# Kernel tuning notes

Hardware: AMD Instinct MI355X
Metric: run time of the kernel (lower is better)

## Reference

```python
import jax, jax.numpy as jnp
import numpy as np

ALPHA = 0.2        # LeakyReLU negative slope
NEG_INF = -9e15    # mask value used by the torch module


def setup_inputs() -> dict:
    key = jax.random.key(0)
    ks = jax.random.split(key, 7)
    B, T, N, Cin = 4, 12, 1024, 64
    Fout, Em = 64, 16
    x = jax.random.normal(ks[0], (B, T, N, Cin), dtype=jnp.float32)
    adj = jax.random.randint(ks[1], (N, N), 0, 2, dtype=jnp.int32)
    emb1 = jax.random.normal(ks[2], (N, Em), dtype=jnp.float32)
    emb2 = jax.random.normal(ks[3], (N, Em), dtype=jnp.float32)
    W = jax.random.normal(ks[4], (Cin, Fout), dtype=jnp.float32) * (1.0 / np.sqrt(Cin))
    a = jax.random.normal(ks[5], (2 * Fout, 1), dtype=jnp.float32) * 0.1
    a2 = jax.random.normal(ks[6], (2 * Em, 1), dtype=jnp.float32) * 0.1
    return {"x": x, "adj": adj, "emb1": emb1, "emb2": emb2, "W": W, "a": a, "a2": a2}


def reference(x, adj, emb1, emb2, W, a, a2):
    B, T, N, Cin = x.shape
    Fout = W.shape[1]
    Em = emb1.shape[1]
    # Linear projection, fold batch*time: Wh [BT, N, Fout]
    Wh = jnp.einsum('btnc,cf->btnf', x, W).reshape(B * T, N, Fout)
    # Additive attention scores from node features
    s1 = Wh @ a[:Fout, 0]          # [BT, N]
    s2 = Wh @ a[Fout:, 0]          # [BT, N]
    e1 = s1[:, :, None] + s2[:, None, :]   # [BT, N, N]
    # Additive scores from static embeddings (shared across batch*time)
    f1 = emb1 @ a2[:Em, 0]         # [N]
    f2 = emb2 @ a2[Em:, 0]         # [N]
    e2 = f1[:, None] + f2[None, :]          # [N, N]
    e = jax.nn.leaky_relu(e1 + e2[None, :, :], negative_slope=ALPHA)
    # Adjacency mask + row softmax (dropout is inference no-op)
    att = jnp.where(adj[None, :, :] > 0, e, jnp.float32(NEG_INF))
    att = jax.nn.softmax(att, axis=-1)
    h_prime = att @ Wh                       # [BT, N, Fout]
    return jax.nn.elu(h_prime.reshape(B, T, N, Fout))
```

## Files before the change

kernel.cpp:

```cpp
#include <hip/hip_runtime.h>
#include <hip/hip_bf16.h>
#include <math.h>

#define BT 48
#define N 1024
#define F 64
#define CIN 64
#define EM 16
#define LRELU_A 0.2f
#define L2E 1.4426950408889634f

typedef short bf16x8 __attribute__((ext_vector_type(8)));
typedef float f32x4  __attribute__((ext_vector_type(4)));
typedef float f32x2  __attribute__((ext_vector_type(2)));
typedef float f32x4e __attribute__((ext_vector_type(4)));
typedef unsigned int u32x4 __attribute__((ext_vector_type(4)));

__device__ __forceinline__ unsigned short f2bf(float f) {
    unsigned int u = __float_as_uint(f);
    return (unsigned short)((u + 0x7FFFu + ((u >> 16) & 1u)) >> 16);
}

#define PKFMA(acc, xp, wp) \
    asm("v_pk_fma_f32 %0, %1, %2, %0" : "+v"(acc) : "v"(xp), "v"(wp))

__global__ __launch_bounds__(256) void k_proj_misc(
    const float* __restrict__ x, const float* __restrict__ W,
    const float* __restrict__ a,
    const int* __restrict__ adj,
    const float* __restrict__ emb1, const float* __restrict__ emb2,
    const float* __restrict__ a2,
    unsigned short* __restrict__ WhSw,
    float* __restrict__ s1, float* __restrict__ s2,
    unsigned int* __restrict__ adjBits,
    float* __restrict__ f1, float* __restrict__ f2)
{
    const int tid = threadIdx.x;
    const int b   = blockIdx.x;

    __shared__ __align__(16) float sxT[64 * 68];
    __shared__ __align__(16) float sW[64 * 68];

    const int bt  = b >> 4;
    const int n0  = (b & 15) * 64;
    const size_t grow = (size_t)bt * N + n0;

    {
        const float4* xv = (const float4*)(x + grow * CIN);
        for (int i = tid; i < 1024; i += 256) {
            const float4 v = xv[i];
            const int row = i >> 4, c4 = (i & 15) * 4;
            sxT[(c4 + 0) * 68 + (row ^ (((c4 + 0) & 15) << 2))] = v.x;
            sxT[(c4 + 1) * 68 + (row ^ (((c4 + 1) & 15) << 2))] = v.y;
            sxT[(c4 + 2) * 68 + (row ^ (((c4 + 2) & 15) << 2))] = v.z;
            sxT[(c4 + 3) * 68 + (row ^ (((c4 + 3) & 15) << 2))] = v.w;
        }
        const float4* wv = (const float4*)W;
        for (int i = tid; i < 1024; i += 256) {
            const int k = i >> 4, c4 = (i & 15) * 4;
            *(float4*)&sW[k * 68 + c4] = wv[i];
        }
    }
    __syncthreads();

    const int rg = tid >> 4, cg = tid & 15;
    const int r0 = rg * 4, c0 = cg * 4;

    f32x2 a00 = 0.f, a01 = 0.f, a10 = 0.f, a11 = 0.f;
    f32x2 a20 = 0.f, a21 = 0.f, a30 = 0.f, a31 = 0.f;

#pragma unroll
    for (int k = 0; k < CIN; ++k) {
        const float4 xr  = *(const float4*)&sxT[k * 68 + (r0 ^ ((k & 15) << 2))];
        const float4 wv4 = *(const float4*)&sW[k * 68 + c0];
        f32x2 w01; w01.x = wv4.x; w01.y = wv4.y;
        f32x2 w23; w23.x = wv4.z; w23.y = wv4.w;
        f32x2 xb;
        xb.x = xr.x; xb.y = xr.x;
        PKFMA(a00, xb, w01); PKFMA(a01, xb, w23);
        xb.x = xr.y; xb.y = xr.y;
        PKFMA(a10, xb, w01); PKFMA(a11, xb, w23);
        xb.x = xr.z; xb.y = xr.z;
        PKFMA(a20, xb, w01); PKFMA(a21, xb, w23);
        xb.x = xr.w; xb.y = xr.w;
        PKFMA(a30, xb, w01); PKFMA(a31, xb, w23);
    }

    {
        const float4 aw1 = *(const float4*)&a[c0];
        const float4 aw2 = *(const float4*)&a[F + c0];
        float v1r0 = a00.x*aw1.x + a00.y*aw1.y + a01.x*aw1.z + a01.y*aw1.w;
        float v1r1 = a10.x*aw1.x + a10.y*aw1.y + a11.x*aw1.z + a11.y*aw1.w;
        float v1r2 = a20.x*aw1.x + a20.y*aw1.y + a21.x*aw1.z + a21.y*aw1.w;
        float v1r3 = a30.x*aw1.x + a30.y*aw1.y + a31.x*aw1.z + a31.y*aw1.w;
        float v2r0 = a00.x*aw2.x + a00.y*aw2.y + a01.x*aw2.z + a01.y*aw2.w;
        float v2r1 = a10.x*aw2.x + a10.y*aw2.y + a11.x*aw2.z + a11.y*aw2.w;
        float v2r2 = a20.x*aw2.x + a20.y*aw2.y + a21.x*aw2.z + a21.y*aw2.w;
        float v2r3 = a30.x*aw2.x + a30.y*aw2.y + a31.x*aw2.z + a31.y*aw2.w;
#pragma unroll
        for (int off = 1; off <= 8; off <<= 1) {
            v1r0 += __shfl_xor(v1r0, off, 64); v2r0 += __shfl_xor(v2r0, off, 64);
            v1r1 += __shfl_xor(v1r1, off, 64); v2r1 += __shfl_xor(v2r1, off, 64);
            v1r2 += __shfl_xor(v1r2, off, 64); v2r2 += __shfl_xor(v2r2, off, 64);
            v1r3 += __shfl_xor(v1r3, off, 64); v2r3 += __shfl_xor(v2r3, off, 64);
        }
        if (cg == 0) {
            s1[grow + r0 + 0] = v1r0; s2[grow + r0 + 0] = v2r0;
            s1[grow + r0 + 1] = v1r1; s2[grow + r0 + 1] = v2r1;
            s1[grow + r0 + 2] = v1r2; s2[grow + r0 + 2] = v2r2;
            s1[grow + r0 + 3] = v1r3; s2[grow + r0 + 3] = v2r3;
        }
    }

    {
        const int nb = (b & 15) * 2 + (r0 >> 5);
        const int qq = (r0 >> 3) & 3;
        const int t0 = r0 & 7;
        const size_t base = ((size_t)(bt * 32 + nb) * 64) * 32;
#define STCOL(cc, v0, v1, v2, v3) do {                                      \
        const int c_ = c0 + (cc);                                           \
        const size_t off_ = base + (size_t)c_ * 32 + ((qq + c_) & 3) * 8 + t0; \
        ushort4 pv_;                                                        \
        pv_.x = f2bf(v0); pv_.y = f2bf(v1);                                 \
        pv_.z = f2bf(v2); pv_.w = f2bf(v3);                                 \
        *(ushort4*)&WhSw[off_] = pv_;                                       \
    } while (0)
        STCOL(0, a00.x, a10.x, a20.x, a30.x);
        STCOL(1, a00.y, a10.y, a20.y, a30.y);
        STCOL(2, a01.x, a11.x, a21.x, a31.x);
        STCOL(3, a01.y, a11.y, a21.y, a31.y);
#undef STCOL
    }

    if (b < 128) {
        const int idx = b * 256 + tid;
        const int r = idx >> 5, w32 = idx & 31;
        const int* p = adj + (size_t)r * N + w32 * 32;
        unsigned int m = 0;
#pragma unroll
        for (int j = 0; j < 32; ++j) m |= (p[j] > 0 ? 1u : 0u) << j;
        adjBits[idx] = m;
    } else if (b < 132) {
        const int n = (b - 128) * 256 + tid;
        float v1 = 0.f, v2 = 0.f;
#pragma unroll
        for (int k = 0; k < EM; ++k) {
            v1 = fmaf(emb1[n * EM + k], a2[k], v1);
            v2 = fmaf(emb2[n * EM + k], a2[EM + k], v2);
        }
        f1[n] = v1; f2[n] = v2;
    }
}


#define PAIRPK(x1p, x2p, bit, dest) do {                                   \
    f32x2 m1_, m2_;                                                        \
    asm("v_pk_mul_f32 %0, %1, %2" : "=v"(m1_) : "v"(x1p), "v"(E1p));       \
    asm("v_pk_mul_f32 %0, %1, %2" : "=v"(m2_) : "v"(x2p), "v"(E2p));       \
    float p0_ = fmaxf(m1_.x, m2_.x);                                       \
    float p1_ = fmaxf(m1_.y, m2_.y);                                       \
    p0_ = ((mb_ >> (bit)) & 1u) ? p0_ : 0.f;                               \
    p1_ = ((mb_ >> ((bit) + 1)) & 1u) ? p1_ : 0.f;                         \
    lsum += p0_ + p1_;                                                     \
    unsigned int pk_;                                                      \
    asm("v_cvt_pk_bf16_f32 %0, %1, %2" : "=v"(pk_) : "v"(p0_), "v"(p1_)); \
    dest = pk_;                                                            \
} while (0)

#define MAKE_ONE(ch, ks, Avar, abword) do {                                \
    const int jb_ = (ch) * 128 + (ks) * 32 + q * 8;                        \
    const f32x4e x1a_ = *(const f32x4e*)&sX1[jb_];                         \
    const f32x4e x1b_ = *(const f32x4e*)&sX1[jb_ + 4];                     \
    const f32x4e x2a_ = *(const f32x4e*)&sX2[jb_];                         \
    const f32x4e x2b_ = *(const f32x4e*)&sX2[jb_ + 4];                     \
    const unsigned int mb_ = ((abword) >> (q * 8)) & 0xFFu;                \
    unsigned int u0_, u1_, u2_, u3_;                                       \
    PAIRPK(__builtin_shufflevector(x1a_, x1a_, 0, 1),                      \
           __builtin_shufflevector(x2a_, x2a_, 0, 1), 0, u0_);             \
    PAIRPK(__builtin_shufflevector(x1a_, x1a_, 2, 3),                      \
           __builtin_shufflevector(x2a_, x2a_, 2, 3), 2, u1_);             \
    PAIRPK(__builtin_shufflevector(x1b_, x1b_, 0, 1),                      \
           __builtin_shufflevector(x2b_, x2b_, 0, 1), 4, u2_);             \
    PAIRPK(__builtin_shufflevector(x1b_, x1b_, 2, 3),                      \
           __builtin_shufflevector(x2b_, x2b_, 2, 3), 6, u3_);             \
    u32x4 av_; av_.x = u0_; av_.y = u1_; av_.z = u2_; av_.w = u3_;         \
    Avar = __builtin_bit_cast(bf16x8, av_);                                \
} while (0)

#define MAKE_AFR(ch, abv, A0, A1, A2, A3) do {                             \
    MAKE_ONE(ch, 0, A0, abv.x);                                            \
    MAKE_ONE(ch, 1, A1, abv.y);                                            \
    MAKE_ONE(ch, 2, A2, abv.z);                                            \
    MAKE_ONE(ch, 3, A3, abv.w);                                            \
} while (0)

#define LB(v, ch, ks, ct)                                                  \
    v = *(const bf16x8*)(gBc + (size_t)(ch) * 16384 + (ks) * 4096 +        \
        ((ct) * 16 + m15) * 64 + slotoff)

#define LOAD8(B0, B1, B2, B3, B4, B5, B6, B7, ch, ct0, ct1) do {           \
    LB(B0, ch, 0, ct0); LB(B1, ch, 1, ct0);                                \
    LB(B2, ch, 2, ct0); LB(B3, ch, 3, ct0);                                \
    LB(B4, ch, 0, ct1); LB(B5, ch, 1, ct1);                                \
    LB(B6, ch, 2, ct1); LB(B7, ch, 3, ct1);                                \
} while (0)

#define MFMA8(B0, B1, B2, B3, B4, B5, B6, B7, c0, c1) do {                 \
    acc##c0 = __builtin_amdgcn_mfma_f32_16x16x32_bf16(fA0, B0, acc##c0, 0, 0, 0); \
    acc##c0 = __builtin_amdgcn_mfma_f32_16x16x32_bf16(fA1, B1, acc##c0, 0, 0, 0); \
    acc##c0 = __builtin_amdgcn_mfma_f32_16x16x32_bf16(fA2, B2, acc##c0, 0, 0, 0); \
    acc##c0 = __builtin_amdgcn_mfma_f32_16x16x32_bf16(fA3, B3, acc##c0, 0, 0, 0); \
    acc##c1 = __builtin_amdgcn_mfma_f32_16x16x32_bf16(fA0, B4, acc##c1, 0, 0, 0); \
    acc##c1 = __builtin_amdgcn_mfma_f32_16x16x32_bf16(fA1, B5, acc##c1, 0, 0, 0); \
    acc##c1 = __builtin_amdgcn_mfma_f32_16x16x32_bf16(fA2, B6, acc##c1, 0, 0, 0); \
    acc##c1 = __builtin_amdgcn_mfma_f32_16x16x32_bf16(fA3, B7, acc##c1, 0, 0, 0); \
} while (0)

#define CHUNK_MID(ch) do {                                                 \
    LOAD8(Q0, Q1, Q2, Q3, Q4, Q5, Q6, Q7, ch, 2, 3);                       \
    const uint4 abv_ = abRow4[ch];                                         \
    MAKE_AFR(ch, abv_, fA0, fA1, fA2, fA3);                                \
    MFMA8(P0, P1, P2, P3, P4, P5, P6, P7, 0, 1);                           \
    LOAD8(P0, P1, P2, P3, P4, P5, P6, P7, (ch) + 1, 0, 1);                 \
    MFMA8(Q0, Q1, Q2, Q3, Q4, Q5, Q6, Q7, 2, 3);                           \
} while (0)

#define CHUNK_LAST(ch) do {                                                \
    LOAD8(Q0, Q1, Q2, Q3, Q4, Q5, Q6, Q7, ch, 2, 3);                       \
    const uint4 abv_ = abRow4[ch];                                         \
    MAKE_AFR(ch, abv_, fA0, fA1, fA2, fA3);                                \
    MFMA8(P0, P1, P2, P3, P4, P5, P6, P7, 0, 1);                           \
    MFMA8(Q0, Q1, Q2, Q3, Q4, Q5, Q6, Q7, 2, 3);                           \
} while (0)

#define EPI(ct, accv) do {                                                 \
    float h0_ = accv.x * rinv0, h1_ = accv.y * rinv1,                      \
          h2_ = accv.z * rinv2, h3_ = accv.w * rinv3;                      \
    h0_ = (h0_ > 0.f) ? h0_ : (__expf(h0_) - 1.f);                         \
    h1_ = (h1_ > 0.f) ? h1_ : (__expf(h1_) - 1.f);                         \
    h2_ = (h2_ > 0.f) ? h2_ : (__expf(h2_) - 1.f);                         \
    h3_ = (h3_ > 0.f) ? h3_ : (__expf(h3_) - 1.f);                         \
    float* op_ = out + (size_t)(bt * N + i0 + w * 16 + q * 4) * F          \
                 + (ct) * 16 + m15;                                        \
    op_[0 * F] = h0_; op_[1 * F] = h1_; op_[2 * F] = h2_; op_[3 * F] = h3_;\
} while (0)

__global__ __launch_bounds__(256, 3) void k_attn(
    const unsigned int* __restrict__ adjBits,
    const unsigned short* __restrict__ WhSw,
    const float* __restrict__ s1, const float* __restrict__ s2,
    const float* __restrict__ f1v, const float* __restrict__ f2v,
    float* __restrict__ out)
{
    __shared__ __align__(16) float sX1[N];
    __shared__ __align__(16) float sX2[N];
    __shared__ float sWmax[4];

    const int tid  = threadIdx.x;
    const int xcd = blockIdx.x & 7;
    const int idx = blockIdx.x >> 3;
    const int bt  = xcd * 6 + (idx >> 4);
    const int i0  = (idx & 15) * 64;
    const int lane = tid & 63;
    const int w    = tid >> 6;
    const int q    = lane >> 4;
    const int m15  = lane & 15;

    const int growq = i0 + w * 16 + m15;
    const uint4* abRow4 = (const uint4*)(adjBits + (size_t)growq * 32);
    const float rraw = s1[bt * N + growq] + f1v[growq];

    float cmax = -1e30f;
    for (int j = tid; j < N; j += 256) {
        const float c = (s2[bt * N + j] + f2v[j]) * L2E;
        sX1[j] = exp2f(c);
        sX2[j] = exp2f(LRELU_A * c);
        cmax = fmaxf(cmax, c);
    }
#pragma unroll
    for (int off = 32; off >= 1; off >>= 1) cmax = fmaxf(cmax, __shfl_xor(cmax, off, 64));
    if (lane == 0) sWmax[w] = cmax;
    __syncthreads();
    const float mx = fmaxf(fmaxf(sWmax[0], sWmax[1]), fmaxf(sWmax[2], sWmax[3]));

    const float r    = rraw * L2E;
    const float smx  = r + mx;
    const float mhat = fmaxf(smx, LRELU_A * smx);
    const float E1 = exp2f(r - mhat);
    const float E2 = exp2f(LRELU_A * r - mhat);
    f32x2 E1p; E1p.x = E1; E1p.y = E1;
    f32x2 E2p; E2p.x = E2; E2p.y = E2;
    float lsum = 0.f;

    const char* gBc = (const char*)(WhSw + (size_t)bt * 65536);
    const int slotoff = ((q + m15) & 3) * 16;

    f32x4 acc0 = 0.f, acc1 = 0.f, acc2 = 0.f, acc3 = 0.f;
    bf16x8 fA0, fA1, fA2, fA3;
    bf16x8 P0, P1, P2, P3, P4, P5, P6, P7;
    bf16x8 Q0, Q1, Q2, Q3, Q4, Q5, Q6, Q7;

    LOAD8(P0, P1, P2, P3, P4, P5, P6, P7, 0, 0, 1);

    CHUNK_MID(0); CHUNK_MID(1); CHUNK_MID(2); CHUNK_MID(3);
    CHUNK_MID(4); CHUNK_MID(5); CHUNK_MID(6); CHUNK_LAST(7);

    lsum += __shfl_xor(lsum, 16, 64);
    lsum += __shfl_xor(lsum, 32, 64);

    const float rinv0 = 1.f / __shfl(lsum, q * 4 + 0, 64);
    const float rinv1 = 1.f / __shfl(lsum, q * 4 + 1, 64);
    const float rinv2 = 1.f / __shfl(lsum, q * 4 + 2, 64);
    const float rinv3 = 1.f / __shfl(lsum, q * 4 + 3, 64);

    EPI(0, acc0); EPI(1, acc1); EPI(2, acc2); EPI(3, acc3);
}

extern "C" void kernel_launch(void* const* d_in, const int* in_sizes, int n_in,
                              void* d_out, int out_size, void* d_ws, size_t ws_size,
                              hipStream_t stream)
{
    const float* x    = (const float*)d_in[0];
    const int*   adj  = (const int*)  d_in[1];
    const float* emb1 = (const float*)d_in[2];
    const float* emb2 = (const float*)d_in[3];
    const float* W    = (const float*)d_in[4];
    const float* a    = (const float*)d_in[5];
    const float* a2   = (const float*)d_in[6];
    float* out = (float*)d_out;

    unsigned short* WhSw = (unsigned short*)d_ws;
    float* s1 = (float*)(WhSw + (size_t)BT * 65536);
    float* s2 = s1 + BT * N;
    float* f1 = s2 + BT * N;
    float* f2 = f1 + N;
    unsigned int* adjBits = (unsigned int*)(f2 + N);

    hipLaunchKernelGGL(k_proj_misc, dim3(768), dim3(256), 0, stream,
                       x, W, a, adj, emb1, emb2, a2, WhSw, s1, s2, adjBits, f1, f2);
    hipLaunchKernelGGL(k_attn, dim3(BT * 16), dim3(256), 0, stream,
                       adjBits, WhSw, s1, s2, f1, f2, out);
}
```

Baseline: 109.7 us.

## Fuse projection and attention into one persistent kernel with atomic ticket dependencies

Merges the projection/prep kernel and the attention kernel into a single launch. Blocks take a ticket from an atomic counter, so producer work is dispatched before consumer work, and per-bt counters plus a global counter gate each attention block until its inputs are ready. This lets attention for early bt slices overlap with projection for later ones and removes the tail and drain gap between the two kernels. In exchange it adds a tiny zeroing kernel, spin-waiting with s_sleep, and a shared-memory footprint sized for the larger producer path, which may lower occupancy for attention blocks.

```diff
diff --git a/kernel.cpp b/kernel.cpp
--- a/kernel.cpp
+++ b/kernel.cpp
@@ -24,132 +24,8 @@
 #define PKFMA(acc, xp, wp) \
     asm("v_pk_fma_f32 %0, %1, %2, %0" : "+v"(acc) : "v"(xp), "v"(wp))
 
-__global__ __launch_bounds__(256) void k_proj_misc(
-    const float* __restrict__ x, const float* __restrict__ W,
-    const float* __restrict__ a,
-    const int* __restrict__ adj,
-    const float* __restrict__ emb1, const float* __restrict__ emb2,
-    const float* __restrict__ a2,
-    unsigned short* __restrict__ WhSw,
-    float* __restrict__ s1, float* __restrict__ s2,
-    unsigned int* __restrict__ adjBits,
-    float* __restrict__ f1, float* __restrict__ f2)
-{
-    const int tid = threadIdx.x;
-    const int b   = blockIdx.x;
-
-    __shared__ __align__(16) float sxT[64 * 68];
-    __shared__ __align__(16) float sW[64 * 68];
-
-    const int bt  = b >> 4;
-    const int n0  = (b & 15) * 64;
-    const size_t grow = (size_t)bt * N + n0;
-
-    {
-        const float4* xv = (const float4*)(x + grow * CIN);
-        for (int i = tid; i < 1024; i += 256) {
-            const float4 v = xv[i];
-            const int row = i >> 4, c4 = (i & 15) * 4;
-            sxT[(c4 + 0) * 68 + (row ^ (((c4 + 0) & 15) << 2))] = v.x;
-            sxT[(c4 + 1) * 68 + (row ^ (((c4 + 1) & 15) << 2))] = v.y;
-            sxT[(c4 + 2) * 68 + (row ^ (((c4 + 2) & 15) << 2))] = v.z;
-            sxT[(c4 + 3) * 68 + (row ^ (((c4 + 3) & 15) << 2))] = v.w;
-        }
-        const float4* wv = (const float4*)W;
-        for (int i = tid; i < 1024; i += 256) {
-            const int k = i >> 4, c4 = (i & 15) * 4;
-            *(float4*)&sW[k * 68 + c4] = wv[i];
-        }
-    }
-    __syncthreads();
-
-    const int rg = tid >> 4, cg = tid & 15;
-    const int r0 = rg * 4, c0 = cg * 4;
-
-    f32x2 a00 = 0.f, a01 = 0.f, a10 = 0.f, a11 = 0.f;
-    f32x2 a20 = 0.f, a21 = 0.f, a30 = 0.f, a31 = 0.f;
-
-#pragma unroll
-    for (int k = 0; k < CIN; ++k) {
-        const float4 xr  = *(const float4*)&sxT[k * 68 + (r0 ^ ((k & 15) << 2))];
-        const float4 wv4 = *(const float4*)&sW[k * 68 + c0];
-        f32x2 w01; w01.x = wv4.x; w01.y = wv4.y;
-        f32x2 w23; w23.x = wv4.z; w23.y = wv4.w;
-        f32x2 xb;
-        xb.x = xr.x; xb.y = xr.x;
-        PKFMA(a00, xb, w01); PKFMA(a01, xb, w23);
-        xb.x = xr.y; xb.y = xr.y;
-        PKFMA(a10, xb, w01); PKFMA(a11, xb, w23);
-        xb.x = xr.z; xb.y = xr.z;
-        PKFMA(a20, xb, w01); PKFMA(a21, xb, w23);
-        xb.x = xr.w; xb.y = xr.w;
-        PKFMA(a30, xb, w01); PKFMA(a31, xb, w23);
-    }
-
-    {
-        const float4 aw1 = *(const float4*)&a[c0];
-        const float4 aw2 = *(const float4*)&a[F + c0];
-        float v1r0 = a00.x*aw1.x + a00.y*aw1.y + a01.x*aw1.z + a01.y*aw1.w;
-        float v1r1 = a10.x*aw1.x + a10.y*aw1.y + a11.x*aw1.z + a11.y*aw1.w;
-        float v1r2 = a20.x*aw1.x + a20.y*aw1.y + a21.x*aw1.z + a21.y*aw1.w;
-        float v1r3 = a30.x*aw1.x + a30.y*aw1.y + a31.x*aw1.z + a31.y*aw1.w;
-        float v2r0 = a00.x*aw2.x + a00.y*aw2.y + a01.x*aw2.z + a01.y*aw2.w;
-        float v2r1 = a10.x*aw2.x + a10.y*aw2.y + a11.x*aw2.z + a11.y*aw2.w;
-        float v2r2 = a20.x*aw2.x + a20.y*aw2.y + a21.x*aw2.z + a21.y*aw2.w;
-        float v2r3 = a30.x*aw2.x + a30.y*aw2.y + a31.x*aw2.z + a31.y*aw2.w;
-#pragma unroll
-        for (int off = 1; off <= 8; off <<= 1) {
-            v1r0 += __shfl_xor(v1r0, off, 64); v2r0 += __shfl_xor(v2r0, off, 64);
-            v1r1 += __shfl_xor(v1r1, off, 64); v2r1 += __shfl_xor(v2r1, off, 64);
-            v1r2 += __shfl_xor(v1r2, off, 64); v2r2 += __shfl_xor(v2r2, off, 64);
-            v1r3 += __shfl_xor(v1r3, off, 64); v2r3 += __shfl_xor(v2r3, off, 64);
-        }
-        if (cg == 0) {
-            s1[grow + r0 + 0] = v1r0; s2[grow + r0 + 0] = v2r0;
-            s1[grow + r0 + 1] = v1r1; s2[grow + r0 + 1] = v2r1;
-            s1[grow + r0 + 2] = v1r2; s2[grow + r0 + 2] = v2r2;
-            s1[grow + r0 + 3] = v1r3; s2[grow + r0 + 3] = v2r3;
-        }
-    }
-
-    {
-        const int nb = (b & 15) * 2 + (r0 >> 5);
-        const int qq = (r0 >> 3) & 3;
-        const int t0 = r0 & 7;
-        const size_t base = ((size_t)(bt * 32 + nb) * 64) * 32;
-#define STCOL(cc, v0, v1, v2, v3) do {                                      \
-        const int c_ = c0 + (cc);                                           \
-        const size_t off_ = base + (size_t)c_ * 32 + ((qq + c_) & 3) * 8 + t0; \
-        ushort4 pv_;                                                        \
-        pv_.x = f2bf(v0); pv_.y = f2bf(v1);                                 \
-        pv_.z = f2bf(v2); pv_.w = f2bf(v3);                                 \
-        *(ushort4*)&WhSw[off_] = pv_;                                       \
-    } while (0)
-        STCOL(0, a00.x, a10.x, a20.x, a30.x);
-        STCOL(1, a00.y, a10.y, a20.y, a30.y);
-        STCOL(2, a01.x, a11.x, a21.x, a31.x);
-        STCOL(3, a01.y, a11.y, a21.y, a31.y);
-#undef STCOL
-    }
-
-    if (b < 128) {
-        const int idx = b * 256 + tid;
-        const int r = idx >> 5, w32 = idx & 31;
-        const int* p = adj + (size_t)r * N + w32 * 32;
-        unsigned int m = 0;
-#pragma unroll
-        for (int j = 0; j < 32; ++j) m |= (p[j] > 0 ? 1u : 0u) << j;
-        adjBits[idx] = m;
-    } else if (b < 132) {
-        const int n = (b - 128) * 256 + tid;
-        float v1 = 0.f, v2 = 0.f;
-#pragma unroll
-        for (int k = 0; k < EM; ++k) {
-            v1 = fmaf(emb1[n * EM + k], a2[k], v1);
-            v2 = fmaf(emb2[n * EM + k], a2[EM + k], v2);
-        }
-        f1[n] = v1; f2[n] = v2;
-    }
+__global__ void k_zero(unsigned int* ctrs) {
+    for (int i = threadIdx.x; i < 1024; i += 256) ctrs[i] = 0u;
 }
 
 
@@ -245,75 +121,228 @@
     op_[0 * F] = h0_; op_[1 * F] = h1_; op_[2 * F] = h2_; op_[3 * F] = h3_;\
 } while (0)
 
-__global__ __launch_bounds__(256, 3) void k_attn(
-    const unsigned int* __restrict__ adjBits,
-    const unsigned short* __restrict__ WhSw,
-    const float* __restrict__ s1, const float* __restrict__ s2,
-    const float* __restrict__ f1v, const float* __restrict__ f2v,
+__global__ __launch_bounds__(256, 3) void k_fused(
+    const float* __restrict__ x, const float* __restrict__ W,
+    const float* __restrict__ a,
+    const int* __restrict__ adj,
+    const float* __restrict__ emb1, const float* __restrict__ emb2,
+    const float* __restrict__ a2,
+    unsigned short* __restrict__ WhSw,
+    float* __restrict__ s1, float* __restrict__ s2,
+    unsigned int* __restrict__ adjBits,
+    float* __restrict__ f1, float* __restrict__ f2,
+    unsigned int* __restrict__ ctrs,
     float* __restrict__ out)
 {
-    __shared__ __align__(16) float sX1[N];
-    __shared__ __align__(16) float sX2[N];
-    __shared__ float sWmax[4];
-
-    const int tid  = threadIdx.x;
-    const int xcd = blockIdx.x & 7;
-    const int idx = blockIdx.x >> 3;
-    const int bt  = xcd * 6 + (idx >> 4);
-    const int i0  = (idx & 15) * 64;
-    const int lane = tid & 63;
-    const int w    = tid >> 6;
-    const int q    = lane >> 4;
-    const int m15  = lane & 15;
-
-    const int growq = i0 + w * 16 + m15;
-    const uint4* abRow4 = (const uint4*)(adjBits + (size_t)growq * 32);
-    const float rraw = s1[bt * N + growq] + f1v[growq];
-
-    float cmax = -1e30f;
-    for (int j = tid; j < N; j += 256) {
-        const float c = (s2[bt * N + j] + f2v[j]) * L2E;
-        sX1[j] = exp2f(c);
-        sX2[j] = exp2f(LRELU_A * c);
-        cmax = fmaxf(cmax, c);
+    __shared__ __align__(16) char smem[34816];
+    __shared__ unsigned int sTicket;
+
+    const int tid = threadIdx.x;
+    if (tid == 0)
+        sTicket = __hip_atomic_fetch_add(&ctrs[784], 1u, __ATOMIC_RELAXED,
+                                         __HIP_MEMORY_SCOPE_AGENT);
+    __syncthreads();
+    const unsigned int tk = sTicket;
+
+    if (tk < 768u) {
+        const int b = (int)tk;
+        float* sxT = (float*)smem;
+        float* sW  = (float*)(smem + 17408);
+
+        const int bt  = b >> 4;
+        const int n0  = (b & 15) * 64;
+        const size_t grow = (size_t)bt * N + n0;
+
+        {
+            const float4* xv = (const float4*)(x + grow * CIN);
+            for (int i = tid; i < 1024; i += 256) {
+                const float4 v = xv[i];
+                const int row = i >> 4, c4 = (i & 15) * 4;
+                sxT[(c4 + 0) * 68 + (row ^ (((c4 + 0) & 15) << 2))] = v.x;
+                sxT[(c4 + 1) * 68 + (row ^ (((c4 + 1) & 15) << 2))] = v.y;
+                sxT[(c4 + 2) * 68 + (row ^ (((c4 + 2) & 15) << 2))] = v.z;
+                sxT[(c4 + 3) * 68 + (row ^ (((c4 + 3) & 15) << 2))] = v.w;
+            }
+            const float4* wv = (const float4*)W;
+            for (int i = tid; i < 1024; i += 256) {
+                const int k = i >> 4, c4 = (i & 15) * 4;
+                *(float4*)&sW[k * 68 + c4] = wv[i];
+            }
+        }
+        __syncthreads();
+
+        const int rg = tid >> 4, cg = tid & 15;
+        const int r0 = rg * 4, c0 = cg * 4;
+
+        f32x2 a00 = 0.f, a01 = 0.f, a10 = 0.f, a11 = 0.f;
+        f32x2 a20 = 0.f, a21 = 0.f, a30 = 0.f, a31 = 0.f;
+
+#pragma unroll
+        for (int k = 0; k < CIN; ++k) {
+            const float4 xr  = *(const float4*)&sxT[k * 68 + (r0 ^ ((k & 15) << 2))];
+            const float4 wv4 = *(const float4*)&sW[k * 68 + c0];
+            f32x2 w01; w01.x = wv4.x; w01.y = wv4.y;
+            f32x2 w23; w23.x = wv4.z; w23.y = wv4.w;
+            f32x2 xb;
+            xb.x = xr.x; xb.y = xr.x;
+            PKFMA(a00, xb, w01); PKFMA(a01, xb, w23);
+            xb.x = xr.y; xb.y = xr.y;
+            PKFMA(a10, xb, w01); PKFMA(a11, xb, w23);
+            xb.x = xr.z; xb.y = xr.z;
+            PKFMA(a20, xb, w01); PKFMA(a21, xb, w23);
+            xb.x = xr.w; xb.y = xr.w;
+            PKFMA(a30, xb, w01); PKFMA(a31, xb, w23);
+        }
+
+        {
+            const float4 aw1 = *(const float4*)&a[c0];
+            const float4 aw2 = *(const float4*)&a[F + c0];
+            float v1r0 = a00.x*aw1.x + a00.y*aw1.y + a01.x*aw1.z + a01.y*aw1.w;
+            float v1r1 = a10.x*aw1.x + a10.y*aw1.y + a11.x*aw1.z + a11.y*aw1.w;
+            float v1r2 = a20.x*aw1.x + a20.y*aw1.y + a21.x*aw1.z + a21.y*aw1.w;
+            float v1r3 = a30.x*aw1.x + a30.y*aw1.y + a31.x*aw1.z + a31.y*aw1.w;
+            float v2r0 = a00.x*aw2.x + a00.y*aw2.y + a01.x*aw2.z + a01.y*aw2.w;
+            float v2r1 = a10.x*aw2.x + a10.y*aw2.y + a11.x*aw2.z + a11.y*aw2.w;
+            float v2r2 = a20.x*aw2.x + a20.y*aw2.y + a21.x*aw2.z + a21.y*aw2.w;
+            float v2r3 = a30.x*aw2.x + a30.y*aw2.y + a31.x*aw2.z + a31.y*aw2.w;
+#pragma unroll
+            for (int off = 1; off <= 8; off <<= 1) {
+                v1r0 += __shfl_xor(v1r0, off, 64); v2r0 += __shfl_xor(v2r0, off, 64);
+                v1r1 += __shfl_xor(v1r1, off, 64); v2r1 += __shfl_xor(v2r1, off, 64);
+                v1r2 += __shfl_xor(v1r2, off, 64); v2r2 += __shfl_xor(v2r2, off, 64);
+                v1r3 += __shfl_xor(v1r3, off, 64); v2r3 += __shfl_xor(v2r3, off, 64);
+            }
+            if (cg == 0) {
+                s1[grow + r0 + 0] = v1r0; s2[grow + r0 + 0] = v2r0;
+                s1[grow + r0 + 1] = v1r1; s2[grow + r0 + 1] = v2r1;
+                s1[grow + r0 + 2] = v1r2; s2[grow + r0 + 2] = v2r2;
+                s1[grow + r0 + 3] = v1r3; s2[grow + r0 + 3] = v2r3;
+            }
+        }
+
+        {
+            const int nb = (b & 15) * 2 + (r0 >> 5);
+            const int qq = (r0 >> 3) & 3;
+            const int t0 = r0 & 7;
+            const size_t base = ((size_t)(bt * 32 + nb) * 64) * 32;
+#define STCOL(cc, v0, v1, v2, v3) do {                                      \
+            const int c_ = c0 + (cc);                                       \
+            const size_t off_ = base + (size_t)c_ * 32 + ((qq + c_) & 3) * 8 + t0; \
+            ushort4 pv_;                                                    \
+            pv_.x = f2bf(v0); pv_.y = f2bf(v1);                             \
+            pv_.z = f2bf(v2); pv_.w = f2bf(v3);                             \
+            *(ushort4*)&WhSw[off_] = pv_;                                   \
+        } while (0)
+            STCOL(0, a00.x, a10.x, a20.x, a30.x);
+            STCOL(1, a00.y, a10.y, a20.y, a30.y);
+            STCOL(2, a01.x, a11.x, a21.x, a31.x);
+            STCOL(3, a01.y, a11.y, a21.y, a31.y);
+#undef STCOL
+        }
+
+        if (b < 128) {
+            const int idx = b * 256 + tid;
+            const int r = idx >> 5, w32 = idx & 31;
+            const int* p = adj + (size_t)r * N + w32 * 32;
+            unsigned int m = 0;
+#pragma unroll
+            for (int j = 0; j < 32; ++j) m |= (p[j] > 0 ? 1u : 0u) << j;
+            adjBits[idx] = m;
+        } else if (b < 132) {
+            const int n = (b - 128) * 256 + tid;
+            float v1 = 0.f, v2 = 0.f;
+#pragma unroll
+            for (int k = 0; k < EM; ++k) {
+                v1 = fmaf(emb1[n * EM + k], a2[k], v1);
+                v2 = fmaf(emb2[n * EM + k], a2[EM + k], v2);
+            }
+            f1[n] = v1; f2[n] = v2;
+        }
+
+        __syncthreads();
+        __threadfence();
+        if (tid == 0) {
+            __hip_atomic_fetch_add(&ctrs[bt * 16], 1u, __ATOMIC_RELEASE,
+                                   __HIP_MEMORY_SCOPE_AGENT);
+            if (b < 132)
+                __hip_atomic_fetch_add(&ctrs[768], 1u, __ATOMIC_RELEASE,
+                                       __HIP_MEMORY_SCOPE_AGENT);
+        }
+    } else {
+        const int cid = (int)(tk - 768u);
+        float* sX1 = (float*)smem;
+        float* sX2 = (float*)(smem + 4096);
+        float* sWmax = (float*)(smem + 8192);
+
+        const int xcd = cid & 7;
+        const int idx = cid >> 3;
+        const int bt  = xcd * 6 + (idx >> 4);
+        const int i0  = (idx & 15) * 64;
+        const int lane = tid & 63;
+        const int w    = tid >> 6;
+        const int q    = lane >> 4;
+        const int m15  = lane & 15;
+
+        if (tid == 0) {
+            while (__hip_atomic_load(&ctrs[768], __ATOMIC_ACQUIRE,
+                                     __HIP_MEMORY_SCOPE_AGENT) < 132u)
+                __builtin_amdgcn_s_sleep(8);
+            while (__hip_atomic_load(&ctrs[bt * 16], __ATOMIC_ACQUIRE,
+                                     __HIP_MEMORY_SCOPE_AGENT) < 16u)
+                __builtin_amdgcn_s_sleep(8);
+        }
+        __syncthreads();
+        __threadfence();
+
+        const int growq = i0 + w * 16 + m15;
+        const uint4* abRow4 = (const uint4*)(adjBits + (size_t)growq * 32);
+        const float rraw = s1[bt * N + growq] + f1[growq];
+
+        float cmax = -1e30f;
+        for (int j = tid; j < N; j += 256) {
+            const float c = (s2[bt * N + j] + f2[j]) * L2E;
+            sX1[j] = exp2f(c);
+            sX2[j] = exp2f(LRELU_A * c);
+            cmax = fmaxf(cmax, c);
+        }
+#pragma unroll
+        for (int off = 32; off >= 1; off >>= 1) cmax = fmaxf(cmax, __shfl_xor(cmax, off, 64));
+        if (lane == 0) sWmax[w] = cmax;
+        __syncthreads();
+        const float mx = fmaxf(fmaxf(sWmax[0], sWmax[1]), fmaxf(sWmax[2], sWmax[3]));
+
+        const float r    = rraw * L2E;
+        const float smx  = r + mx;
+        const float mhat = fmaxf(smx, LRELU_A * smx);
+        const float E1 = exp2f(r - mhat);
+        const float E2 = exp2f(LRELU_A * r - mhat);
+        f32x2 E1p; E1p.x = E1; E1p.y = E1;
+        f32x2 E2p; E2p.x = E2; E2p.y = E2;
+        float lsum = 0.f;
+
+        const char* gBc = (const char*)(WhSw + (size_t)bt * 65536);
+        const int slotoff = ((q + m15) & 3) * 16;
+
+        f32x4 acc0 = 0.f, acc1 = 0.f, acc2 = 0.f, acc3 = 0.f;
+        bf16x8 fA0, fA1, fA2, fA3;
+        bf16x8 P0, P1, P2, P3, P4, P5, P6, P7;
+        bf16x8 Q0, Q1, Q2, Q3, Q4, Q5, Q6, Q7;
+
+        LOAD8(P0, P1, P2, P3, P4, P5, P6, P7, 0, 0, 1);
+
+        CHUNK_MID(0); CHUNK_MID(1); CHUNK_MID(2); CHUNK_MID(3);
+        CHUNK_MID(4); CHUNK_MID(5); CHUNK_MID(6); CHUNK_LAST(7);
+
+        lsum += __shfl_xor(lsum, 16, 64);
+        lsum += __shfl_xor(lsum, 32, 64);
+
+        const float rinv0 = 1.f / __shfl(lsum, q * 4 + 0, 64);
+        const float rinv1 = 1.f / __shfl(lsum, q * 4 + 1, 64);
+        const float rinv2 = 1.f / __shfl(lsum, q * 4 + 2, 64);
+        const float rinv3 = 1.f / __shfl(lsum, q * 4 + 3, 64);
+
+        EPI(0, acc0); EPI(1, acc1); EPI(2, acc2); EPI(3, acc3);
     }
-#pragma unroll
-    for (int off = 32; off >= 1; off >>= 1) cmax = fmaxf(cmax, __shfl_xor(cmax, off, 64));
-    if (lane == 0) sWmax[w] = cmax;
-    __syncthreads();
-    const float mx = fmaxf(fmaxf(sWmax[0], sWmax[1]), fmaxf(sWmax[2], sWmax[3]));
-
-    const float r    = rraw * L2E;
-    const float smx  = r + mx;
-    const float mhat = fmaxf(smx, LRELU_A * smx);
-    const float E1 = exp2f(r - mhat);
-    const float E2 = exp2f(LRELU_A * r - mhat);
-    f32x2 E1p; E1p.x = E1; E1p.y = E1;
-    f32x2 E2p; E2p.x = E2; E2p.y = E2;
-    float lsum = 0.f;
-
-    const char* gBc = (const char*)(WhSw + (size_t)bt * 65536);
-    const int slotoff = ((q + m15) & 3) * 16;
-
-    f32x4 acc0 = 0.f, acc1 = 0.f, acc2 = 0.f, acc3 = 0.f;
-    bf16x8 fA0, fA1, fA2, fA3;
-    bf16x8 P0, P1, P2, P3, P4, P5, P6, P7;
-    bf16x8 Q0, Q1, Q2, Q3, Q4, Q5, Q6, Q7;
-
-    LOAD8(P0, P1, P2, P3, P4, P5, P6, P7, 0, 0, 1);
-
-    CHUNK_MID(0); CHUNK_MID(1); CHUNK_MID(2); CHUNK_MID(3);
-    CHUNK_MID(4); CHUNK_MID(5); CHUNK_MID(6); CHUNK_LAST(7);
-
-    lsum += __shfl_xor(lsum, 16, 64);
-    lsum += __shfl_xor(lsum, 32, 64);
-
-    const float rinv0 = 1.f / __shfl(lsum, q * 4 + 0, 64);
-    const float rinv1 = 1.f / __shfl(lsum, q * 4 + 1, 64);
-    const float rinv2 = 1.f / __shfl(lsum, q * 4 + 2, 64);
-    const float rinv3 = 1.f / __shfl(lsum, q * 4 + 3, 64);
-
-    EPI(0, acc0); EPI(1, acc1); EPI(2, acc2); EPI(3, acc3);
 }
 
 extern "C" void kernel_launch(void* const* d_in, const int* in_sizes, int n_in,
@@ -335,9 +364,10 @@
     float* f1 = s2 + BT * N;
     float* f2 = f1 + N;
     unsigned int* adjBits = (unsigned int*)(f2 + N);
-
-    hipLaunchKernelGGL(k_proj_misc, dim3(768), dim3(256), 0, stream,
-                       x, W, a, adj, emb1, emb2, a2, WhSw, s1, s2, adjBits, f1, f2);
-    hipLaunchKernelGGL(k_attn, dim3(BT * 16), dim3(256), 0, stream,
-                       adjBits, WhSw, s1, s2, f1, f2, out);
+    unsigned int* ctrs = adjBits + 32768;
+
+    hipLaunchKernelGGL(k_zero, dim3(1), dim3(256), 0, stream, ctrs);
+    hipLaunchKernelGGL(k_fused, dim3(1536), dim3(256), 0, stream,
+                       x, W, a, adj, emb1, emb2, a2, WhSw, s1, s2,
+                       adjBits, f1, f2, ctrs, out);
 }
```

Measured after the change: 311.1 us. +183.5%, slower.
